# Kernel tuning notes

Measured on AMD Instinct MI355X. Metric: run time of the kernel, lower is better.

The kernel has to match this reference:

```python
import jax, jax.numpy as jnp
import numpy as np

NUM_ATTRS = 8    # A: number of attribute names in attr_map
NUM_VALS = 16    # V: number of distinct values per attribute


def setup_inputs() -> dict:
    key = jax.random.key(0)
    k1, k2 = jax.random.split(key)
    B, D = 2_000_000, 8
    predictions = jax.random.normal(k1, (B, D), dtype=jnp.float32)
    attr_vals = jax.random.randint(k2, (B, NUM_ATTRS), 0, NUM_VALS, dtype=jnp.int32)
    return {"predictions": predictions, "attr_vals": attr_vals}


def reference(predictions, attr_vals):
    B, A = attr_vals.shape
    V = NUM_VALS
    # per-node mean of sigmoid probs; stacking rows then .mean() == mean of per-node means
    per_node = jnp.mean(jax.nn.sigmoid(predictions), axis=1)  # [B]
    # flatten (attr, value) groups into A*V segments
    seg_ids = (attr_vals + jnp.arange(A, dtype=attr_vals.dtype)[None, :] * V).reshape(-1)  # [B*A]
    vals = jnp.broadcast_to(per_node[:, None], (B, A)).reshape(-1)  # [B*A]
    sums = jax.ops.segment_sum(vals, seg_ids, num_segments=A * V)
    counts = jax.ops.segment_sum(jnp.ones_like(vals), seg_ids, num_segments=A * V)
    means = (sums / jnp.maximum(counts, 1.0)).reshape(A, V)      # [A, V]
    present = (counts > 0).reshape(A, V)                          # [A, V]
    # pairwise squared diffs of group means within each attribute (i < j)
    diff = means[:, :, None] - means[:, None, :]                  # [A, V, V]
    triu = jnp.triu(jnp.ones((V, V), dtype=bool), k=1)
    pair_mask = present[:, :, None] & present[:, None, :] & triu[None, :, :]
    total_loss = jnp.sum(jnp.where(pair_mask, diff * diff, 0.0))
    num_comparisons = jnp.sum(pair_mask)
    return jnp.where(num_comparisons > 0, total_loss / num_comparisons, 0.0)
```

## Files before the change

kernel.cpp:

```cpp
#include <hip/hip_runtime.h>

#define NA 8
#define NV 16
#define NS (NA * NV)
#define FIX_SHIFT 43
#define FIX_MASK ((1ULL << FIX_SHIFT) - 1)
#define FIX_SCALE 2147483648.0f

__global__ __launch_bounds__(256) void k1_accum(
    const float* __restrict__ preds,
    const int*   __restrict__ attrs,
    unsigned long long* __restrict__ partials,
    int B, int nb)
{
    __shared__ unsigned long long h[NS];
    for (int i = threadIdx.x; i < NS; i += 256) h[i] = 0ULL;
    __syncthreads();

    const int stride = nb * 256;
    for (int r = blockIdx.x * 256 + threadIdx.x; r < B; r += stride) {
        const float4* p4 = (const float4*)(preds + (size_t)r * NA);
        float4 p0 = p4[0];
        float4 p1 = p4[1];

        float s = __builtin_amdgcn_rcpf(1.0f + __expf(-p0.x))
                + __builtin_amdgcn_rcpf(1.0f + __expf(-p0.y))
                + __builtin_amdgcn_rcpf(1.0f + __expf(-p0.z))
                + __builtin_amdgcn_rcpf(1.0f + __expf(-p0.w))
                + __builtin_amdgcn_rcpf(1.0f + __expf(-p1.x))
                + __builtin_amdgcn_rcpf(1.0f + __expf(-p1.y))
                + __builtin_amdgcn_rcpf(1.0f + __expf(-p1.z))
                + __builtin_amdgcn_rcpf(1.0f + __expf(-p1.w));
        float per_node = s * 0.125f;
        unsigned int fixed = (unsigned int)(per_node * FIX_SCALE);
        unsigned long long add = (1ULL << FIX_SHIFT) | (unsigned long long)fixed;

        const int4* a4 = (const int4*)(attrs + (size_t)r * NA);
        int4 a0 = a4[0];
        int4 a1 = a4[1];

        atomicAdd(&h[0 * NV + a0.x], add);
        atomicAdd(&h[1 * NV + a0.y], add);
        atomicAdd(&h[2 * NV + a0.z], add);
        atomicAdd(&h[3 * NV + a0.w], add);
        atomicAdd(&h[4 * NV + a1.x], add);
        atomicAdd(&h[5 * NV + a1.y], add);
        atomicAdd(&h[6 * NV + a1.z], add);
        atomicAdd(&h[7 * NV + a1.w], add);
    }
    __syncthreads();

    if (threadIdx.x < NS) {
        partials[(size_t)threadIdx.x * nb + blockIdx.x] = h[threadIdx.x];
    }
}

__global__ __launch_bounds__(256) void k2_reduce(
    const unsigned long long* __restrict__ partials,
    double* __restrict__ means,
    int*    __restrict__ pres,
    int nb)
{
    const int s = blockIdx.x;
    unsigned long long sum = 0ULL;
    unsigned int cnt = 0u;
    for (int b = threadIdx.x; b < nb; b += 256) {
        unsigned long long p = partials[(size_t)s * nb + b];
        cnt += (unsigned int)(p >> FIX_SHIFT);
        sum += (p & FIX_MASK);
    }
    for (int off = 32; off > 0; off >>= 1) {
        sum += __shfl_down(sum, off, 64);
        cnt += __shfl_down(cnt, off, 64);
    }
    __shared__ unsigned long long ws_[4];
    __shared__ unsigned int wc_[4];
    const int wave = threadIdx.x >> 6;
    if ((threadIdx.x & 63) == 0) { ws_[wave] = sum; wc_[wave] = cnt; }
    __syncthreads();
    if (threadIdx.x == 0) {
        unsigned long long S = ws_[0] + ws_[1] + ws_[2] + ws_[3];
        unsigned int C = wc_[0] + wc_[1] + wc_[2] + wc_[3];
        means[s] = C ? ((double)S * (1.0 / (double)FIX_SCALE)) / (double)C : 0.0;
        pres[s]  = C ? 1 : 0;
    }
}

__global__ __launch_bounds__(128) void k3_finalize(
    const double* __restrict__ means,
    const int*    __restrict__ pres,
    float* __restrict__ out)
{
    __shared__ double s_mean[NS];
    __shared__ int    s_pres[NS];
    const int t = threadIdx.x;
    s_mean[t] = means[t];
    s_pres[t] = pres[t];
    __syncthreads();

    const int a = t >> 4;
    const int i = t & (NV - 1);
    double loss = 0.0;
    int    ncmp = 0;
    if (s_pres[t]) {
        const double mi = s_mean[t];
        for (int j = i + 1; j < NV; ++j) {
            const int sj = a * NV + j;
            if (s_pres[sj]) {
                const double d = mi - s_mean[sj];
                loss += d * d;
                ncmp += 1;
            }
        }
    }
    for (int off = 32; off > 0; off >>= 1) {
        loss += __shfl_down(loss, off, 64);
        ncmp += __shfl_down(ncmp, off, 64);
    }
    __shared__ double w_loss[2];
    __shared__ int    w_ncmp[2];
    const int wave = t >> 6;
    if ((t & 63) == 0) { w_loss[wave] = loss; w_ncmp[wave] = ncmp; }
    __syncthreads();
    if (t == 0) {
        const double total = w_loss[0] + w_loss[1];
        const int    n     = w_ncmp[0] + w_ncmp[1];
        out[0] = (n > 0) ? (float)(total / (double)n) : 0.0f;
    }
}

extern "C" void kernel_launch(void* const* d_in, const int* in_sizes, int n_in,
                              void* d_out, int out_size, void* d_ws, size_t ws_size,
                              hipStream_t stream) {
    const float* preds = (const float*)d_in[0];
    const int*   attrs = (const int*)d_in[1];
    float*       out   = (float*)d_out;

    const int B = in_sizes[1] / NA;

    const size_t tail = NS * sizeof(double) + NS * sizeof(int);
    int nb = 1024;
    if (ws_size < (size_t)NS * 1024 * sizeof(unsigned long long) + tail) nb = 512;

    unsigned long long* partials = (unsigned long long*)d_ws;
    double* means = (double*)((char*)d_ws + (size_t)NS * nb * sizeof(unsigned long long));
    int*    pres  = (int*)(means + NS);

    k1_accum<<<nb, 256, 0, stream>>>(preds, attrs, partials, B, nb);
    k2_reduce<<<NS, 256, 0, stream>>>(partials, means, pres, nb);
    k3_finalize<<<1, 128, 0, stream>>>(means, pres, out);
}
```

Measured before the change: 148.9 us.

## Pack attribute pairs into joint histograms to halve shared atomics

Instead of eight LDS atomics per row (one per attribute), pairs of attributes are combined into a 256-bin joint histogram, so each row does four atomics into four 256-bin histograms. The per-attribute marginals are recovered in the finalize kernel by summing the rows or columns of each joint histogram. This trades fewer, less contended atomics for an eightfold larger partials buffer, more reduction blocks in the second kernel, and a larger grid (up to 2048 blocks). Larger histograms also spread updates across more bins, which lowers same-address conflicts.

```diff
diff --git a/kernel.cpp b/kernel.cpp
--- a/kernel.cpp
+++ b/kernel.cpp
@@ -3,6 +3,8 @@
 #define NA 8
 #define NV 16
 #define NS (NA * NV)
+#define NP 4
+#define NJ 256
 #define FIX_SHIFT 43
 #define FIX_MASK ((1ULL << FIX_SHIFT) - 1)
 #define FIX_SCALE 2147483648.0f
@@ -13,8 +15,8 @@
     unsigned long long* __restrict__ partials,
     int B, int nb)
 {
-    __shared__ unsigned long long h[NS];
-    for (int i = threadIdx.x; i < NS; i += 256) h[i] = 0ULL;
+    __shared__ unsigned long long h[NP * NJ];
+    for (int i = threadIdx.x; i < NP * NJ; i += 256) h[i] = 0ULL;
     __syncthreads();
 
     const int stride = nb * 256;
@@ -39,33 +41,29 @@
         int4 a0 = a4[0];
         int4 a1 = a4[1];
 
-        atomicAdd(&h[0 * NV + a0.x], add);
-        atomicAdd(&h[1 * NV + a0.y], add);
-        atomicAdd(&h[2 * NV + a0.z], add);
-        atomicAdd(&h[3 * NV + a0.w], add);
-        atomicAdd(&h[4 * NV + a1.x], add);
-        atomicAdd(&h[5 * NV + a1.y], add);
-        atomicAdd(&h[6 * NV + a1.z], add);
-        atomicAdd(&h[7 * NV + a1.w], add);
+        atomicAdd(&h[0 * NJ + ((a0.x << 4) | a0.y)], add);
+        atomicAdd(&h[1 * NJ + ((a0.z << 4) | a0.w)], add);
+        atomicAdd(&h[2 * NJ + ((a1.x << 4) | a1.y)], add);
+        atomicAdd(&h[3 * NJ + ((a1.z << 4) | a1.w)], add);
     }
     __syncthreads();
 
-    if (threadIdx.x < NS) {
-        partials[(size_t)threadIdx.x * nb + blockIdx.x] = h[threadIdx.x];
+    for (int i = threadIdx.x; i < NP * NJ; i += 256) {
+        partials[(size_t)i * nb + blockIdx.x] = h[i];
     }
 }
 
 __global__ __launch_bounds__(256) void k2_reduce(
     const unsigned long long* __restrict__ partials,
-    double* __restrict__ means,
-    int*    __restrict__ pres,
+    unsigned long long* __restrict__ jsum,
+    unsigned int*       __restrict__ jcnt,
     int nb)
 {
-    const int s = blockIdx.x;
+    const int e = blockIdx.x;
     unsigned long long sum = 0ULL;
     unsigned int cnt = 0u;
     for (int b = threadIdx.x; b < nb; b += 256) {
-        unsigned long long p = partials[(size_t)s * nb + b];
+        unsigned long long p = partials[(size_t)e * nb + b];
         cnt += (unsigned int)(p >> FIX_SHIFT);
         sum += (p & FIX_MASK);
     }
@@ -79,33 +77,49 @@
     if ((threadIdx.x & 63) == 0) { ws_[wave] = sum; wc_[wave] = cnt; }
     __syncthreads();
     if (threadIdx.x == 0) {
-        unsigned long long S = ws_[0] + ws_[1] + ws_[2] + ws_[3];
-        unsigned int C = wc_[0] + wc_[1] + wc_[2] + wc_[3];
-        means[s] = C ? ((double)S * (1.0 / (double)FIX_SCALE)) / (double)C : 0.0;
-        pres[s]  = C ? 1 : 0;
+        jsum[e] = ws_[0] + ws_[1] + ws_[2] + ws_[3];
+        jcnt[e] = wc_[0] + wc_[1] + wc_[2] + wc_[3];
     }
 }
 
 __global__ __launch_bounds__(128) void k3_finalize(
-    const double* __restrict__ means,
-    const int*    __restrict__ pres,
+    const unsigned long long* __restrict__ jsum,
+    const unsigned int*       __restrict__ jcnt,
     float* __restrict__ out)
 {
     __shared__ double s_mean[NS];
     __shared__ int    s_pres[NS];
+
     const int t = threadIdx.x;
-    s_mean[t] = means[t];
-    s_pres[t] = pres[t];
+    const int a = t >> 4;
+    const int v = t & (NV - 1);
+    const int p = a >> 1;
+
+    unsigned long long S = 0ULL;
+    unsigned int C = 0u;
+    if ((a & 1) == 0) {
+        for (int j = 0; j < NV; ++j) {
+            const int e = p * NJ + (v << 4) + j;
+            S += jsum[e]; C += jcnt[e];
+        }
+    } else {
+        for (int i = 0; i < NV; ++i) {
+            const int e = p * NJ + (i << 4) + v;
+            S += jsum[e]; C += jcnt[e];
+        }
+    }
+    s_pres[t] = (C > 0u) ? 1 : 0;
+    s_mean[t] = (C > 0u)
+        ? ((double)S * (1.0 / (double)FIX_SCALE)) / (double)C : 0.0;
     __syncthreads();
 
-    const int a = t >> 4;
-    const int i = t & (NV - 1);
+    const int i0 = v;
     double loss = 0.0;
     int    ncmp = 0;
     if (s_pres[t]) {
         const double mi = s_mean[t];
-        for (int j = i + 1; j < NV; ++j) {
-            const int sj = a * NV + j;
+        for (int j = i0 + 1; j < NV; ++j) {
+            const int sj = (a << 4) + j;
             if (s_pres[sj]) {
                 const double d = mi - s_mean[sj];
                 loss += d * d;
@@ -138,15 +152,19 @@
 
     const int B = in_sizes[1] / NA;
 
-    const size_t tail = NS * sizeof(double) + NS * sizeof(int);
-    int nb = 1024;
-    if (ws_size < (size_t)NS * 1024 * sizeof(unsigned long long) + tail) nb = 512;
+    const size_t tail = (size_t)NP * NJ * (sizeof(unsigned long long) + sizeof(unsigned int));
+    int nb = 2048;
+    while (nb > 256 &&
+           (size_t)NP * NJ * nb * sizeof(unsigned long long) + tail > ws_size) {
+        nb >>= 1;
+    }
 
     unsigned long long* partials = (unsigned long long*)d_ws;
-    double* means = (double*)((char*)d_ws + (size_t)NS * nb * sizeof(unsigned long long));
-    int*    pres  = (int*)(means + NS);
+    unsigned long long* jsum = (unsigned long long*)((char*)d_ws +
+        (size_t)NP * NJ * nb * sizeof(unsigned long long));
+    unsigned int* jcnt = (unsigned int*)(jsum + NP * NJ);
 
     k1_accum<<<nb, 256, 0, stream>>>(preds, attrs, partials, B, nb);
-    k2_reduce<<<NS, 256, 0, stream>>>(partials, means, pres, nb);
-    k3_finalize<<<1, 128, 0, stream>>>(means, pres, out);
+    k2_reduce<<<NP * NJ, 256, 0, stream>>>(partials, jsum, jcnt, nb);
+    k3_finalize<<<1, 128, 0, stream>>>(jsum, jcnt, out);
 }
```

After: 172.1 us. 15.5% more time.
